# Kernel tuning notes

Hardware: AMD Instinct MI355X
Metric: run time of the kernel (lower is better)

The kernel has to match this reference:

```python
import jax, jax.numpy as jnp
import numpy as np

B, N, D = 16, 1024, 768
H = 12
HD = D // H           # 64
NUM_BUCKETS = 49      # iRPE 'product' buckets, shared across heads
SCALE = HD ** -0.5


def setup_inputs() -> dict:
    key = jax.random.key(0)
    k1, k2, k3, k4, k5, k6 = jax.random.split(key, 6)
    x = jax.random.normal(k1, (B, N, D), dtype=jnp.float32)
    qkv_w = jax.random.normal(k2, (3 * D, D), dtype=jnp.float32) * 0.02
    rpe_table = jax.random.normal(k3, (NUM_BUCKETS, HD), dtype=jnp.float32) * 0.02
    rp_bucket = jax.random.randint(k4, (N, N), 0, NUM_BUCKETS, dtype=jnp.int32)
    proj_w = jax.random.normal(k5, (D, D), dtype=jnp.float32) * 0.02
    proj_b = jax.random.normal(k6, (D,), dtype=jnp.float32) * 0.02
    return {"x": x, "qkv_w": qkv_w, "rpe_table": rpe_table,
            "rp_bucket": rp_bucket, "proj_w": proj_w, "proj_b": proj_b}


def reference(x, qkv_w, rpe_table, rp_bucket, proj_w, proj_b):
    b, n, d = x.shape
    # qkv projection (no bias), split into q,k,v of shape [B,H,N,HD]
    qkv = (x @ qkv_w.T).reshape(b, n, 3, H, HD)
    qkv = jnp.transpose(qkv, (2, 0, 3, 1, 4))
    q, k, v = qkv[0], qkv[1], qkv[2]
    q = q * SCALE
    # full attention scores [B,H,N,N]
    attn = jnp.einsum('bhid,bhjd->bhij', q, k)
    # iRPE contextual bias on keys: project q onto the bucket table, then
    # gather per relative-position bucket: bias[b,h,i,j] = (q @ W^T)[b,h,i,rp_bucket[i,j]]
    bias_all = jnp.einsum('bhid,cd->bhic', q, rpe_table)   # [B,H,N,num_buckets]
    bias = bias_all[:, :, jnp.arange(n)[:, None], rp_bucket]  # [B,H,N,N]
    attn = jax.nn.softmax(attn + bias, axis=-1)
    out = jnp.einsum('bhij,bhjd->bhid', attn, v)            # [B,H,N,HD]
    out = jnp.transpose(out, (0, 2, 1, 3)).reshape(b, n, d)
    return out @ proj_w.T + proj_b
```

## Files before the change

### kernel.cpp

```cpp
#include <hip/hip_runtime.h>

typedef short bf16x8 __attribute__((ext_vector_type(8)));
typedef float f32x4 __attribute__((ext_vector_type(4)));

#define QSCALE 0.1803368801111204f

__device__ __forceinline__ unsigned short f2bf(float f){
  unsigned u = __float_as_uint(f);
  u = (u + 0x7fffu + ((u >> 16) & 1u)) >> 16;
  return (unsigned short)u;
}
__device__ __forceinline__ f32x4 mfma16(bf16x8 a, bf16x8 b, f32x4 c){
  return __builtin_amdgcn_mfma_f32_16x16x32_bf16(a, b, c, 0, 0, 0);
}
__device__ __forceinline__ void gload_lds16(const void* g, void* l){
  __builtin_amdgcn_global_load_lds((__attribute__((address_space(1))) void*)(g),
                                   (__attribute__((address_space(3))) void*)(l), 16, 0, 0);
}
__device__ __forceinline__ unsigned cvt_pk_bf16(float lo, float hi){
  unsigned r;
  asm("v_cvt_pk_bf16_f32 %0, %1, %2" : "=v"(r) : "v"(lo), "v"(hi));
  return r;
}
__device__ __forceinline__ float exp2_fast(float x){
  float r;
  asm("v_exp_f32 %0, %1" : "=v"(r) : "v"(x));
  return r;
}

__global__ __launch_bounds__(256) void prep_kernel(
    const float* __restrict__ x, const float* __restrict__ qw,
    const float* __restrict__ pw, const int* __restrict__ rp,
    unsigned short* __restrict__ xb, unsigned short* __restrict__ wb,
    unsigned short* __restrict__ pwb, unsigned char* __restrict__ rp8){
  const int T1 = 3145728;
  const int T2 = T1 + 442368;
  const int T3 = T2 + 147456;
  const int T4 = T3 + 262144;
  for (int t = blockIdx.x * 256 + threadIdx.x; t < T4; t += gridDim.x * 256){
    if (t < T3){
      const float4* src; ushort4* dst; int off;
      if (t < T1){ src = (const float4*)x;  dst = (ushort4*)xb;  off = t; }
      else if (t < T2){ src = (const float4*)qw; dst = (ushort4*)wb;  off = t - T1; }
      else { src = (const float4*)pw; dst = (ushort4*)pwb; off = t - T2; }
      float4 v = src[off];
      ushort4 u;
      u.x = f2bf(v.x); u.y = f2bf(v.y); u.z = f2bf(v.z); u.w = f2bf(v.w);
      dst[off] = u;
    } else {
      int off = t - T3;
      int4 v = ((const int4*)rp)[off];
      int row = (off * 4) >> 10;
      int sw = (row & 7) << 4;
      uchar4 u;
      u.x = (unsigned char)((v.x << 1) ^ sw);
      u.y = (unsigned char)((v.y << 1) ^ sw);
      u.z = (unsigned char)((v.z << 1) ^ sw);
      u.w = (unsigned char)((v.w << 1) ^ sw);
      ((uchar4*)rp8)[off] = u;
    }
  }
}

__device__ __forceinline__ void gemm_core(
    const unsigned short* __restrict__ A, const unsigned short* __restrict__ Bm,
    int m0, int n0, int K, unsigned short* As, unsigned short* Bs,
    f32x4 (&acc)[4][4]){
  const int tid = threadIdx.x, lane = tid & 63, wave = tid >> 6;
  const int g = lane >> 4, r16 = lane & 15;
  const int wr = wave >> 1, wc = wave & 1;
  for (int k0 = 0; k0 < K; k0 += 32){
    __syncthreads();
    #pragma unroll
    for (int j = 0; j < 2; j++){
      int ci = j * 256 + tid;
      int row = ci >> 2, c = ci & 3;
      gload_lds16(A  + (size_t)(m0 + row) * K + k0 + c * 8,
                  (char*)As + (j * 256 + wave * 64) * 16);
      gload_lds16(Bm + (size_t)(n0 + row) * K + k0 + c * 8,
                  (char*)Bs + (j * 256 + wave * 64) * 16);
    }
    __syncthreads();
    bf16x8 a[4], b[4];
    #pragma unroll
    for (int mi = 0; mi < 4; mi++)
      a[mi] = *(const bf16x8*)((const char*)As + (wr * 64 + mi * 16 + r16) * 64 + g * 16);
    #pragma unroll
    for (int ni = 0; ni < 4; ni++)
      b[ni] = *(const bf16x8*)((const char*)Bs + (wc * 64 + ni * 16 + r16) * 64 + g * 16);
    #pragma unroll
    for (int mi = 0; mi < 4; mi++)
      #pragma unroll
      for (int ni = 0; ni < 4; ni++)
        acc[mi][ni] = mfma16(a[mi], b[ni], acc[mi][ni]);
  }
}

__global__ __launch_bounds__(256) void qkv_gemm(
    const unsigned short* __restrict__ xb, const unsigned short* __restrict__ wb,
    unsigned short* __restrict__ q_s, unsigned short* __restrict__ k_s,
    unsigned short* __restrict__ v_t){
  __shared__ __align__(16) unsigned short As[128 * 32];
  __shared__ __align__(16) unsigned short Bs[128 * 32];
  f32x4 acc[4][4];
  #pragma unroll
  for (int i = 0; i < 4; i++)
    #pragma unroll
    for (int j = 0; j < 4; j++){
      acc[i][j][0] = 0.f; acc[i][j][1] = 0.f; acc[i][j][2] = 0.f; acc[i][j][3] = 0.f;
    }
  const int m0 = blockIdx.y * 128, n0 = blockIdx.x * 128;
  gemm_core(xb, wb, m0, n0, 768, As, Bs, acc);

  const int lane = threadIdx.x & 63, wave = threadIdx.x >> 6;
  const int g = lane >> 4, r16 = lane & 15;
  const int wr = wave >> 1, wc = wave & 1;
  #pragma unroll
  for (int mi = 0; mi < 4; mi++){
    #pragma unroll
    for (int ni = 0; ni < 4; ni++){
      int gcol = n0 + wc * 64 + ni * 16 + r16;
      int sel = gcol / 768;
      int rem = gcol - sel * 768;
      int h = rem >> 6, hd = rem & 63;
      #pragma unroll
      for (int r = 0; r < 4; r++){
        int grow = m0 + wr * 64 + mi * 16 + 4 * g + r;
        int bb = grow >> 10, ii = grow & 1023;
        size_t base = ((size_t)(bb * 12 + h)) << 16;
        float v = acc[mi][ni][r];
        if (sel == 0)      q_s[base + ((size_t)ii << 6) + hd] = f2bf(v * QSCALE);
        else if (sel == 1) k_s[base + ((size_t)ii << 6) + hd] = f2bf(v);
        else               v_t[base + ((size_t)hd << 10) + ii] = f2bf(v);
      }
    }
  }
}

__global__ __launch_bounds__(256) void attn_kernel(
    const unsigned short* __restrict__ q_s, const unsigned short* __restrict__ k_s,
    const unsigned short* __restrict__ v_t, const unsigned char* __restrict__ rp8,
    const float* __restrict__ rpe, unsigned short* __restrict__ ao){
  __shared__ __align__(16) char smem[32768];
  const int tid = threadIdx.x, lane = tid & 63, w = tid >> 6;
  const int g = lane >> 4, r16 = lane & 15;
  const int qb = blockIdx.x, bh = blockIdx.y;
  const size_t bh_base = (size_t)bh << 16;

  const int i_loc = w * 16 + r16;
  const size_t qoff = bh_base + ((size_t)(qb * 64 + i_loc) << 6);
  bf16x8 qf0 = *(const bf16x8*)(q_s + qoff + g * 8);
  bf16x8 qf1 = *(const bf16x8*)(q_s + qoff + 32 + g * 8);

  char* bias_lds = smem + 24576;
  const int s16 = (r16 & 7) << 4;
  #pragma unroll
  for (int jt = 0; jt < 4; jt++){
    int crow = jt * 16 + r16;
    bf16x8 a0, a1;
    #pragma unroll
    for (int e = 0; e < 8; e++){ a0[e] = 0; a1[e] = 0; }
    if (crow < 49){
      const float* rr = rpe + crow * 64 + g * 8;
      float4 x0 = *(const float4*)(rr);
      float4 x1 = *(const float4*)(rr + 4);
      float4 y0 = *(const float4*)(rr + 32);
      float4 y1 = *(const float4*)(rr + 36);
      a0[0]=f2bf(x0.x); a0[1]=f2bf(x0.y); a0[2]=f2bf(x0.z); a0[3]=f2bf(x0.w);
      a0[4]=f2bf(x1.x); a0[5]=f2bf(x1.y); a0[6]=f2bf(x1.z); a0[7]=f2bf(x1.w);
      a1[0]=f2bf(y0.x); a1[1]=f2bf(y0.y); a1[2]=f2bf(y0.z); a1[3]=f2bf(y0.w);
      a1[4]=f2bf(y1.x); a1[5]=f2bf(y1.y); a1[6]=f2bf(y1.z); a1[7]=f2bf(y1.w);
    }
    f32x4 z = {0.f, 0.f, 0.f, 0.f};
    z = mfma16(a0, qf0, z);
    z = mfma16(a1, qf1, z);
    uint2 u; u.x = cvt_pk_bf16(z[0], z[1]); u.y = cvt_pk_bf16(z[2], z[3]);
    *(uint2*)(bias_lds + i_loc * 128 + ((jt * 32 + 8 * g) ^ s16)) = u;
  }

  unsigned short* ks = (unsigned short*)smem;
  unsigned short* vs = (unsigned short*)(smem + 8192);
  char* pbuf = smem + 16384 + w * 2048;
  const char* browb = bias_lds + i_loc * 128;

  const int ci0 = tid, ci1 = 256 + tid;
  const int row0 = ci0 >> 3, sc0 = (ci0 & 7) ^ (row0 & 7);
  const int row1 = ci1 >> 3, sc1 = (ci1 & 7) ^ (row1 & 7);
  const char* kp0 = (const char*)(k_s + bh_base) + row0 * 128 + sc0 * 16;
  const char* kp1 = (const char*)(k_s + bh_base) + row1 * 128 + sc1 * 16;
  const char* vp0 = (const char*)(v_t + bh_base) + row0 * 2048 + sc0 * 16;
  const char* vp1 = (const char*)(v_t + bh_base) + row1 * 2048 + sc1 * 16;
  char* kl0 = (char*)smem + w * 1024;
  char* kl1 = (char*)smem + 4096 + w * 1024;
  char* vl0 = (char*)smem + 8192 + w * 1024;
  char* vl1 = (char*)smem + 12288 + w * 1024;
  const unsigned char* rprow = rp8 + ((size_t)(qb * 64 + i_loc) << 10);

  f32x4 o[4];
  #pragma unroll
  for (int dt = 0; dt < 4; dt++){ o[dt][0]=0.f; o[dt][1]=0.f; o[dt][2]=0.f; o[dt][3]=0.f; }
  float m_i = -INFINITY, l_i = 0.f;

  for (int kb = 0; kb < 16; kb++){
    __syncthreads();
    gload_lds16(kp0, kl0);
    gload_lds16(kp1, kl1);
    gload_lds16(vp0, vl0);
    gload_lds16(vp1, vl1);
    kp0 += 8192; kp1 += 8192; vp0 += 128; vp1 += 128;
    __syncthreads();

    f32x4 st[4];
    #pragma unroll
    for (int jt = 0; jt < 4; jt++){
      int krow = jt * 16 + r16;
      int sw = (krow & 7) << 4;
      bf16x8 ka0 = *(const bf16x8*)((char*)ks + krow * 128 + ((g * 16) ^ sw));
      bf16x8 ka1 = *(const bf16x8*)((char*)ks + krow * 128 + ((64 + g * 16) ^ sw));
      f32x4 z = {0.f, 0.f, 0.f, 0.f};
      z = mfma16(ka0, qf0, z);
      z = mfma16(ka1, qf1, z);
      st[jt] = z;
    }
    #pragma unroll
    for (int jt = 0; jt < 4; jt++){
      unsigned bu = *(const unsigned*)(rprow + kb * 64 + jt * 16 + g * 4);
      st[jt][0] += __uint_as_float((unsigned)*(const unsigned short*)(browb + (bu & 0xff)) << 16);
      st[jt][1] += __uint_as_float((unsigned)*(const unsigned short*)(browb + ((bu >> 8) & 0xff)) << 16);
      st[jt][2] += __uint_as_float((unsigned)*(const unsigned short*)(browb + ((bu >> 16) & 0xff)) << 16);
      st[jt][3] += __uint_as_float((unsigned)*(const unsigned short*)(browb + (bu >> 24)) << 16);
    }
    float tmax = -INFINITY;
    #pragma unroll
    for (int jt = 0; jt < 4; jt++)
      tmax = fmaxf(tmax, fmaxf(fmaxf(st[jt][0], st[jt][1]), fmaxf(st[jt][2], st[jt][3])));
    tmax = fmaxf(tmax, __shfl_xor(tmax, 16));
    tmax = fmaxf(tmax, __shfl_xor(tmax, 32));
    const bool skip = __all(tmax <= m_i + 8.f);
    if (!skip){
      float mnew = fmaxf(m_i, tmax);
      float alpha = exp2_fast(m_i - mnew);
      m_i = mnew;
      l_i *= alpha;
      float af[4];
      #pragma unroll
      for (int r = 0; r < 4; r++) af[r] = __shfl(alpha, 4 * g + r);
      #pragma unroll
      for (int dt = 0; dt < 4; dt++){
        o[dt][0] *= af[0]; o[dt][1] *= af[1]; o[dt][2] *= af[2]; o[dt][3] *= af[3];
      }
    }
    #pragma unroll
    for (int jt = 0; jt < 4; jt++){
      float p0 = exp2_fast(st[jt][0] - m_i);
      float p1 = exp2_fast(st[jt][1] - m_i);
      float p2 = exp2_fast(st[jt][2] - m_i);
      float p3 = exp2_fast(st[jt][3] - m_i);
      l_i += (p0 + p1) + (p2 + p3);
      uint2 u; u.x = cvt_pk_bf16(p0, p1); u.y = cvt_pk_bf16(p2, p3);
      *(uint2*)(pbuf + r16 * 128 + ((jt * 32 + g * 8) ^ ((r16 & 7) << 4))) = u;
    }
    #pragma unroll
    for (int kt = 0; kt < 2; kt++){
      bf16x8 pa = *(const bf16x8*)(pbuf + r16 * 128 + ((kt * 64 + g * 16) ^ ((r16 & 7) << 4)));
      #pragma unroll
      for (int dt = 0; dt < 4; dt++){
        int vrow = dt * 16 + r16;
        bf16x8 vb = *(const bf16x8*)((char*)vs + vrow * 128 + ((kt * 64 + g * 16) ^ ((vrow & 7) << 4)));
        o[dt] = mfma16(pa, vb, o[dt]);
      }
    }
  }

  l_i += __shfl_xor(l_i, 16);
  l_i += __shfl_xor(l_i, 32);
  float lf[4];
  #pragma unroll
  for (int r = 0; r < 4; r++) lf[r] = 1.f / __shfl(l_i, 4 * g + r);
  const int bidx = bh / 12, h = bh - bidx * 12;
  #pragma unroll
  for (int dt = 0; dt < 4; dt++){
    int d = dt * 16 + r16;
    #pragma unroll
    for (int r = 0; r < 4; r++){
      int i = qb * 64 + w * 16 + 4 * g + r;
      ao[(size_t)(bidx * 1024 + i) * 768 + h * 64 + d] = f2bf(o[dt][r] * lf[r]);
    }
  }
}

__global__ __launch_bounds__(256) void proj_gemm(
    const unsigned short* __restrict__ aob, const unsigned short* __restrict__ pwb,
    const float* __restrict__ pb, float* __restrict__ out){
  __shared__ __align__(16) unsigned short As[128 * 32];
  __shared__ __align__(16) unsigned short Bs[128 * 32];
  f32x4 acc[4][4];
  #pragma unroll
  for (int i = 0; i < 4; i++)
    #pragma unroll
    for (int j = 0; j < 4; j++){
      acc[i][j][0] = 0.f; acc[i][j][1] = 0.f; acc[i][j][2] = 0.f; acc[i][j][3] = 0.f;
    }
  const int m0 = blockIdx.y * 128, n0 = blockIdx.x * 128;
  gemm_core(aob, pwb, m0, n0, 768, As, Bs, acc);

  const int lane = threadIdx.x & 63, wave = threadIdx.x >> 6;
  const int g = lane >> 4, r16 = lane & 15;
  const int wr = wave >> 1, wc = wave & 1;
  #pragma unroll
  for (int mi = 0; mi < 4; mi++){
    #pragma unroll
    for (int ni = 0; ni < 4; ni++){
      int gcol = n0 + wc * 64 + ni * 16 + r16;
      float bias = pb[gcol];
      #pragma unroll
      for (int r = 0; r < 4; r++){
        int grow = m0 + wr * 64 + mi * 16 + 4 * g + r;
        out[(size_t)grow * 768 + gcol] = acc[mi][ni][r] + bias;
      }
    }
  }
}

extern "C" void kernel_launch(void* const* d_in, const int* in_sizes, int n_in,
                              void* d_out, int out_size, void* d_ws, size_t ws_size,
                              hipStream_t stream){
  const float* x      = (const float*)d_in[0];
  const float* qkv_w  = (const float*)d_in[1];
  const float* rpe    = (const float*)d_in[2];
  const int*   rp     = (const int*)d_in[3];
  const float* proj_w = (const float*)d_in[4];
  const float* proj_b = (const float*)d_in[5];
  float* out = (float*)d_out;
  char* ws = (char*)d_ws;

  unsigned short* xb  = (unsigned short*)(ws);
  unsigned short* wb  = (unsigned short*)(ws + 25165824);
  unsigned short* pwb = (unsigned short*)(ws + 28704768);
  unsigned char*  rp8 = (unsigned char*) (ws + 29884416);
  unsigned short* q_s = (unsigned short*)(ws + 30932992);
  unsigned short* k_s = (unsigned short*)(ws + 56098816);
  unsigned short* v_t = (unsigned short*)(ws + 81264640);
  unsigned short* aob = (unsigned short*)(ws + 106430464);

  prep_kernel<<<2048, 256, 0, stream>>>(x, qkv_w, proj_w, rp, xb, wb, pwb, rp8);
  qkv_gemm<<<dim3(18, 128), 256, 0, stream>>>(xb, wb, q_s, k_s, v_t);
  attn_kernel<<<dim3(16, 192), 256, 0, stream>>>(q_s, k_s, v_t, rp8, rpe, aob);
  proj_gemm<<<dim3(6, 128), 256, 0, stream>>>(aob, pwb, proj_b, out);
}
```

Baseline: 311.3 us.

## Double-buffer K/V tiles in LDS to overlap loads with attention compute

Grows shared memory from 32KB to 48KB and splits the K/V staging area into two 16KB buffers. The next K/V tile is issued with global_load_lds into the spare buffer while the current tile is consumed, so there is one barrier per iteration instead of two. This aims to hide global load latency behind the QK^T, bias, softmax and PV work. The larger LDS footprint may reduce how many blocks fit per CU.

```diff
diff --git a/kernel.cpp b/kernel.cpp
--- a/kernel.cpp
+++ b/kernel.cpp
@@ -141,7 +141,7 @@
     const unsigned short* __restrict__ q_s, const unsigned short* __restrict__ k_s,
     const unsigned short* __restrict__ v_t, const unsigned char* __restrict__ rp8,
     const float* __restrict__ rpe, unsigned short* __restrict__ ao){
-  __shared__ __align__(16) char smem[32768];
+  __shared__ __align__(16) char smem[49152];
   const int tid = threadIdx.x, lane = tid & 63, w = tid >> 6;
   const int g = lane >> 4, r16 = lane & 15;
   const int qb = blockIdx.x, bh = blockIdx.y;
@@ -152,7 +152,7 @@
   bf16x8 qf0 = *(const bf16x8*)(q_s + qoff + g * 8);
   bf16x8 qf1 = *(const bf16x8*)(q_s + qoff + 32 + g * 8);
 
-  char* bias_lds = smem + 24576;
+  char* bias_lds = smem + 40960;
   const int s16 = (r16 & 7) << 4;
   #pragma unroll
   for (int jt = 0; jt < 4; jt++){
@@ -178,9 +178,7 @@
     *(uint2*)(bias_lds + i_loc * 128 + ((jt * 32 + 8 * g) ^ s16)) = u;
   }
 
-  unsigned short* ks = (unsigned short*)smem;
-  unsigned short* vs = (unsigned short*)(smem + 8192);
-  char* pbuf = smem + 16384 + w * 2048;
+  char* pbuf = smem + 32768 + w * 2048;
   const char* browb = bias_lds + i_loc * 128;
 
   const int ci0 = tid, ci1 = 256 + tid;
@@ -190,10 +188,8 @@
   const char* kp1 = (const char*)(k_s + bh_base) + row1 * 128 + sc1 * 16;
   const char* vp0 = (const char*)(v_t + bh_base) + row0 * 2048 + sc0 * 16;
   const char* vp1 = (const char*)(v_t + bh_base) + row1 * 2048 + sc1 * 16;
-  char* kl0 = (char*)smem + w * 1024;
-  char* kl1 = (char*)smem + 4096 + w * 1024;
-  char* vl0 = (char*)smem + 8192 + w * 1024;
-  char* vl1 = (char*)smem + 12288 + w * 1024;
+  const int kd0 = w * 1024, kd1 = 4096 + w * 1024;
+  const int vd0 = 8192 + w * 1024, vd1 = 12288 + w * 1024;
   const unsigned char* rprow = rp8 + ((size_t)(qb * 64 + i_loc) << 10);
 
   f32x4 o[4];
@@ -201,22 +197,34 @@
   for (int dt = 0; dt < 4; dt++){ o[dt][0]=0.f; o[dt][1]=0.f; o[dt][2]=0.f; o[dt][3]=0.f; }
   float m_i = -INFINITY, l_i = 0.f;
 
+  gload_lds16(kp0, smem + kd0);
+  gload_lds16(kp1, smem + kd1);
+  gload_lds16(vp0, smem + vd0);
+  gload_lds16(vp1, smem + vd1);
+  kp0 += 8192; kp1 += 8192; vp0 += 128; vp1 += 128;
+  __syncthreads();
+
+  int cur = 0;
   for (int kb = 0; kb < 16; kb++){
-    __syncthreads();
-    gload_lds16(kp0, kl0);
-    gload_lds16(kp1, kl1);
-    gload_lds16(vp0, vl0);
-    gload_lds16(vp1, vl1);
-    kp0 += 8192; kp1 += 8192; vp0 += 128; vp1 += 128;
-    __syncthreads();
+    if (kb < 15){
+      char* wbuf = smem + ((cur ^ 1) << 14);
+      gload_lds16(kp0, wbuf + kd0);
+      gload_lds16(kp1, wbuf + kd1);
+      gload_lds16(vp0, wbuf + vd0);
+      gload_lds16(vp1, wbuf + vd1);
+      kp0 += 8192; kp1 += 8192; vp0 += 128; vp1 += 128;
+    }
+    const char* rbuf = smem + (cur << 14);
+    const unsigned short* ks = (const unsigned short*)rbuf;
+    const unsigned short* vs = (const unsigned short*)(rbuf + 8192);
 
     f32x4 st[4];
     #pragma unroll
     for (int jt = 0; jt < 4; jt++){
       int krow = jt * 16 + r16;
       int sw = (krow & 7) << 4;
-      bf16x8 ka0 = *(const bf16x8*)((char*)ks + krow * 128 + ((g * 16) ^ sw));
-      bf16x8 ka1 = *(const bf16x8*)((char*)ks + krow * 128 + ((64 + g * 16) ^ sw));
+      bf16x8 ka0 = *(const bf16x8*)((const char*)ks + krow * 128 + ((g * 16) ^ sw));
+      bf16x8 ka1 = *(const bf16x8*)((const char*)ks + krow * 128 + ((64 + g * 16) ^ sw));
       f32x4 z = {0.f, 0.f, 0.f, 0.f};
       z = mfma16(ka0, qf0, z);
       z = mfma16(ka1, qf1, z);
@@ -266,10 +274,12 @@
       #pragma unroll
       for (int dt = 0; dt < 4; dt++){
         int vrow = dt * 16 + r16;
-        bf16x8 vb = *(const bf16x8*)((char*)vs + vrow * 128 + ((kt * 64 + g * 16) ^ ((vrow & 7) << 4)));
+        bf16x8 vb = *(const bf16x8*)((const char*)vs + vrow * 128 + ((kt * 64 + g * 16) ^ ((vrow & 7) << 4)));
         o[dt] = mfma16(pa, vb, o[dt]);
       }
     }
+    __syncthreads();
+    cur ^= 1;
   }
 
   l_i += __shfl_xor(l_i, 16);
```

New measurement: 324.9 us. +4.4%, slower.

## Widen GEMM K-tile with swizzled LDS and prefetch RPE bias in attention

Applied to the files above, without the earlier changes.

The shared GEMM core now stages 64-wide K tiles, with an XOR swizzle on the LDS layout, and runs two MFMA sub-steps per barrier pair. This halves the number of sync rounds and avoids LDS bank conflicts, at the cost of doubling LDS per block. The attention kernel software-pipelines the rp_bucket index loads and the bias-table lookups one key block ahead, so their latency is hidden behind the QK MFMAs. It also raises wave priority around the MFMA sections. The prefetch adds register pressure (16 extra bias values per thread) and could lower occupancy.

```diff
diff --git a/kernel.cpp b/kernel.cpp
--- a/kernel.cpp
+++ b/kernel.cpp
@@ -69,30 +69,38 @@
   const int tid = threadIdx.x, lane = tid & 63, wave = tid >> 6;
   const int g = lane >> 4, r16 = lane & 15;
   const int wr = wave >> 1, wc = wave & 1;
-  for (int k0 = 0; k0 < K; k0 += 32){
+  for (int k0 = 0; k0 < K; k0 += 64){
     __syncthreads();
     #pragma unroll
-    for (int j = 0; j < 2; j++){
+    for (int j = 0; j < 4; j++){
       int ci = j * 256 + tid;
-      int row = ci >> 2, c = ci & 3;
-      gload_lds16(A  + (size_t)(m0 + row) * K + k0 + c * 8,
+      int row = ci >> 3, c = ci & 7;
+      int sc = c ^ (row & 7);
+      gload_lds16(A  + (size_t)(m0 + row) * K + k0 + sc * 8,
                   (char*)As + (j * 256 + wave * 64) * 16);
-      gload_lds16(Bm + (size_t)(n0 + row) * K + k0 + c * 8,
+      gload_lds16(Bm + (size_t)(n0 + row) * K + k0 + sc * 8,
                   (char*)Bs + (j * 256 + wave * 64) * 16);
     }
     __syncthreads();
-    bf16x8 a[4], b[4];
-    #pragma unroll
-    for (int mi = 0; mi < 4; mi++)
-      a[mi] = *(const bf16x8*)((const char*)As + (wr * 64 + mi * 16 + r16) * 64 + g * 16);
-    #pragma unroll
-    for (int ni = 0; ni < 4; ni++)
-      b[ni] = *(const bf16x8*)((const char*)Bs + (wc * 64 + ni * 16 + r16) * 64 + g * 16);
-    #pragma unroll
-    for (int mi = 0; mi < 4; mi++)
-      #pragma unroll
-      for (int ni = 0; ni < 4; ni++)
-        acc[mi][ni] = mfma16(a[mi], b[ni], acc[mi][ni]);
+    #pragma unroll
+    for (int kk = 0; kk < 2; kk++){
+      bf16x8 a[4], b[4];
+      #pragma unroll
+      for (int mi = 0; mi < 4; mi++){
+        int row = wr * 64 + mi * 16 + r16;
+        a[mi] = *(const bf16x8*)((const char*)As + row * 128 + ((kk * 64 + g * 16) ^ ((row & 7) << 4)));
+      }
+      #pragma unroll
+      for (int ni = 0; ni < 4; ni++){
+        int row = wc * 64 + ni * 16 + r16;
+        b[ni] = *(const bf16x8*)((const char*)Bs + row * 128 + ((kk * 64 + g * 16) ^ ((row & 7) << 4)));
+      }
+      #pragma unroll
+      for (int mi = 0; mi < 4; mi++)
+        #pragma unroll
+        for (int ni = 0; ni < 4; ni++)
+          acc[mi][ni] = mfma16(a[mi], b[ni], acc[mi][ni]);
+    }
   }
 }
 
@@ -100,8 +108,8 @@
     const unsigned short* __restrict__ xb, const unsigned short* __restrict__ wb,
     unsigned short* __restrict__ q_s, unsigned short* __restrict__ k_s,
     unsigned short* __restrict__ v_t){
-  __shared__ __align__(16) unsigned short As[128 * 32];
-  __shared__ __align__(16) unsigned short Bs[128 * 32];
+  __shared__ __align__(16) unsigned short As[128 * 64];
+  __shared__ __align__(16) unsigned short Bs[128 * 64];
   f32x4 acc[4][4];
   #pragma unroll
   for (int i = 0; i < 4; i++)
@@ -201,6 +209,21 @@
   for (int dt = 0; dt < 4; dt++){ o[dt][0]=0.f; o[dt][1]=0.f; o[dt][2]=0.f; o[dt][3]=0.f; }
   float m_i = -INFINITY, l_i = 0.f;
 
+  unsigned buc[4];
+  #pragma unroll
+  for (int jt = 0; jt < 4; jt++)
+    buc[jt] = *(const unsigned*)(rprow + jt * 16 + g * 4);
+  __syncthreads();
+  unsigned bcur[16];
+  #pragma unroll
+  for (int jt = 0; jt < 4; jt++){
+    unsigned bu = buc[jt];
+    bcur[jt*4+0] = *(const unsigned short*)(browb + (bu & 0xff));
+    bcur[jt*4+1] = *(const unsigned short*)(browb + ((bu >> 8) & 0xff));
+    bcur[jt*4+2] = *(const unsigned short*)(browb + ((bu >> 16) & 0xff));
+    bcur[jt*4+3] = *(const unsigned short*)(browb + (bu >> 24));
+  }
+
   for (int kb = 0; kb < 16; kb++){
     __syncthreads();
     gload_lds16(kp0, kl0);
@@ -208,27 +231,45 @@
     gload_lds16(vp0, vl0);
     gload_lds16(vp1, vl1);
     kp0 += 8192; kp1 += 8192; vp0 += 128; vp1 += 128;
+    unsigned bun[4];
+    if (kb < 15){
+      #pragma unroll
+      for (int jt = 0; jt < 4; jt++)
+        bun[jt] = *(const unsigned*)(rprow + (kb + 1) * 64 + jt * 16 + g * 4);
+    }
     __syncthreads();
 
     f32x4 st[4];
+    __builtin_amdgcn_s_setprio(1);
     #pragma unroll
     for (int jt = 0; jt < 4; jt++){
       int krow = jt * 16 + r16;
       int sw = (krow & 7) << 4;
-      bf16x8 ka0 = *(const bf16x8*)((char*)ks + krow * 128 + ((g * 16) ^ sw));
-      bf16x8 ka1 = *(const bf16x8*)((char*)ks + krow * 128 + ((64 + g * 16) ^ sw));
+      bf16x8 ka0 = *(const bf16x8*)((const char*)ks + krow * 128 + ((g * 16) ^ sw));
+      bf16x8 ka1 = *(const bf16x8*)((const char*)ks + krow * 128 + ((64 + g * 16) ^ sw));
       f32x4 z = {0.f, 0.f, 0.f, 0.f};
       z = mfma16(ka0, qf0, z);
       z = mfma16(ka1, qf1, z);
       st[jt] = z;
     }
+    __builtin_amdgcn_s_setprio(0);
+    unsigned bnx[16];
+    if (kb < 15){
+      #pragma unroll
+      for (int jt = 0; jt < 4; jt++){
+        unsigned bu = bun[jt];
+        bnx[jt*4+0] = *(const unsigned short*)(browb + (bu & 0xff));
+        bnx[jt*4+1] = *(const unsigned short*)(browb + ((bu >> 8) & 0xff));
+        bnx[jt*4+2] = *(const unsigned short*)(browb + ((bu >> 16) & 0xff));
+        bnx[jt*4+3] = *(const unsigned short*)(browb + (bu >> 24));
+      }
+    }
     #pragma unroll
     for (int jt = 0; jt < 4; jt++){
-      unsigned bu = *(const unsigned*)(rprow + kb * 64 + jt * 16 + g * 4);
-      st[jt][0] += __uint_as_float((unsigned)*(const unsigned short*)(browb + (bu & 0xff)) << 16);
-      st[jt][1] += __uint_as_float((unsigned)*(const unsigned short*)(browb + ((bu >> 8) & 0xff)) << 16);
-      st[jt][2] += __uint_as_float((unsigned)*(const unsigned short*)(browb + ((bu >> 16) & 0xff)) << 16);
-      st[jt][3] += __uint_as_float((unsigned)*(const unsigned short*)(browb + (bu >> 24)) << 16);
+      st[jt][0] += __uint_as_float(bcur[jt*4+0] << 16);
+      st[jt][1] += __uint_as_float(bcur[jt*4+1] << 16);
+      st[jt][2] += __uint_as_float(bcur[jt*4+2] << 16);
+      st[jt][3] += __uint_as_float(bcur[jt*4+3] << 16);
     }
     float tmax = -INFINITY;
     #pragma unroll
@@ -260,15 +301,21 @@
       uint2 u; u.x = cvt_pk_bf16(p0, p1); u.y = cvt_pk_bf16(p2, p3);
       *(uint2*)(pbuf + r16 * 128 + ((jt * 32 + g * 8) ^ ((r16 & 7) << 4))) = u;
     }
+    __builtin_amdgcn_s_setprio(1);
     #pragma unroll
     for (int kt = 0; kt < 2; kt++){
       bf16x8 pa = *(const bf16x8*)(pbuf + r16 * 128 + ((kt * 64 + g * 16) ^ ((r16 & 7) << 4)));
       #pragma unroll
       for (int dt = 0; dt < 4; dt++){
         int vrow = dt * 16 + r16;
-        bf16x8 vb = *(const bf16x8*)((char*)vs + vrow * 128 + ((kt * 64 + g * 16) ^ ((vrow & 7) << 4)));
+        bf16x8 vb = *(const bf16x8*)((const char*)vs + vrow * 128 + ((kt * 64 + g * 16) ^ ((vrow & 7) << 4)));
         o[dt] = mfma16(pa, vb, o[dt]);
       }
+    }
+    __builtin_amdgcn_s_setprio(0);
+    if (kb < 15){
+      #pragma unroll
+      for (int t = 0; t < 16; t++) bcur[t] = bnx[t];
     }
   }
 
@@ -292,8 +339,8 @@
 __global__ __launch_bounds__(256) void proj_gemm(
     const unsigned short* __restrict__ aob, const unsigned short* __restrict__ pwb,
     const float* __restrict__ pb, float* __restrict__ out){
-  __shared__ __align__(16) unsigned short As[128 * 32];
-  __shared__ __align__(16) unsigned short Bs[128 * 32];
+  __shared__ __align__(16) unsigned short As[128 * 64];
+  __shared__ __align__(16) unsigned short Bs[128 * 64];
   f32x4 acc[4][4];
   #pragma unroll
   for (int i = 0; i < 4; i++)
```

Result: slower. 328.4 us (+5.5%).

## Split RPE bias projection into separate kernel and gather bias from global memory

Applied to the files above, without the earlier changes.

Moves the q·rpe_table bias projection out of the attention kernel into its own bias_gemm kernel, which writes a per-row 64-entry bf16 table into the reused xb workspace. The attention kernel then gathers bias values from global (cached) memory instead of a swizzled LDS region, which shrinks LDS to 24 KB and may raise occupancy. The bucket-index loads are hoisted before the barrier, and s_setprio is placed around the MFMA sections. The cost is an extra kernel launch, an extra global round trip for the bias table, and scattered per-lane global gathers that replace LDS reads.

```diff
diff --git a/kernel.cpp b/kernel.cpp
--- a/kernel.cpp
+++ b/kernel.cpp
@@ -50,13 +50,11 @@
     } else {
       int off = t - T3;
       int4 v = ((const int4*)rp)[off];
-      int row = (off * 4) >> 10;
-      int sw = (row & 7) << 4;
       uchar4 u;
-      u.x = (unsigned char)((v.x << 1) ^ sw);
-      u.y = (unsigned char)((v.y << 1) ^ sw);
-      u.z = (unsigned char)((v.z << 1) ^ sw);
-      u.w = (unsigned char)((v.w << 1) ^ sw);
+      u.x = (unsigned char)(v.x << 1);
+      u.y = (unsigned char)(v.y << 1);
+      u.z = (unsigned char)(v.z << 1);
+      u.w = (unsigned char)(v.w << 1);
       ((uchar4*)rp8)[off] = u;
     }
   }
@@ -137,23 +135,18 @@
   }
 }
 
-__global__ __launch_bounds__(256) void attn_kernel(
-    const unsigned short* __restrict__ q_s, const unsigned short* __restrict__ k_s,
-    const unsigned short* __restrict__ v_t, const unsigned char* __restrict__ rp8,
-    const float* __restrict__ rpe, unsigned short* __restrict__ ao){
-  __shared__ __align__(16) char smem[32768];
+__global__ __launch_bounds__(256) void bias_gemm(
+    const unsigned short* __restrict__ q_s, const float* __restrict__ rpe,
+    unsigned short* __restrict__ bg){
   const int tid = threadIdx.x, lane = tid & 63, w = tid >> 6;
   const int g = lane >> 4, r16 = lane & 15;
   const int qb = blockIdx.x, bh = blockIdx.y;
   const size_t bh_base = (size_t)bh << 16;
-
   const int i_loc = w * 16 + r16;
   const size_t qoff = bh_base + ((size_t)(qb * 64 + i_loc) << 6);
   bf16x8 qf0 = *(const bf16x8*)(q_s + qoff + g * 8);
   bf16x8 qf1 = *(const bf16x8*)(q_s + qoff + 32 + g * 8);
-
-  char* bias_lds = smem + 24576;
-  const int s16 = (r16 & 7) << 4;
+  unsigned short* orow = bg + ((((size_t)bh << 10) + qb * 64 + i_loc) << 6);
   #pragma unroll
   for (int jt = 0; jt < 4; jt++){
     int crow = jt * 16 + r16;
@@ -175,13 +168,29 @@
     z = mfma16(a0, qf0, z);
     z = mfma16(a1, qf1, z);
     uint2 u; u.x = cvt_pk_bf16(z[0], z[1]); u.y = cvt_pk_bf16(z[2], z[3]);
-    *(uint2*)(bias_lds + i_loc * 128 + ((jt * 32 + 8 * g) ^ s16)) = u;
-  }
+    *(uint2*)(orow + jt * 16 + 4 * g) = u;
+  }
+}
+
+__global__ __launch_bounds__(256) void attn_kernel(
+    const unsigned short* __restrict__ q_s, const unsigned short* __restrict__ k_s,
+    const unsigned short* __restrict__ v_t, const unsigned char* __restrict__ rp8,
+    const unsigned short* __restrict__ bg, unsigned short* __restrict__ ao){
+  __shared__ __align__(16) char smem[24576];
+  const int tid = threadIdx.x, lane = tid & 63, w = tid >> 6;
+  const int g = lane >> 4, r16 = lane & 15;
+  const int qb = blockIdx.x, bh = blockIdx.y;
+  const size_t bh_base = (size_t)bh << 16;
+
+  const int i_loc = w * 16 + r16;
+  const size_t qoff = bh_base + ((size_t)(qb * 64 + i_loc) << 6);
+  bf16x8 qf0 = *(const bf16x8*)(q_s + qoff + g * 8);
+  bf16x8 qf1 = *(const bf16x8*)(q_s + qoff + 32 + g * 8);
 
   unsigned short* ks = (unsigned short*)smem;
   unsigned short* vs = (unsigned short*)(smem + 8192);
   char* pbuf = smem + 16384 + w * 2048;
-  const char* browb = bias_lds + i_loc * 128;
+  const char* browb = (const char*)(bg + ((((size_t)bh << 10) + qb * 64 + i_loc) << 6));
 
   const int ci0 = tid, ci1 = 256 + tid;
   const int row0 = ci0 >> 3, sc0 = (ci0 & 7) ^ (row0 & 7);
@@ -208,27 +217,36 @@
     gload_lds16(vp0, vl0);
     gload_lds16(vp1, vl1);
     kp0 += 8192; kp1 += 8192; vp0 += 128; vp1 += 128;
+    unsigned bu0 = *(const unsigned*)(rprow + kb * 64 + g * 4);
+    unsigned bu1 = *(const unsigned*)(rprow + kb * 64 + 16 + g * 4);
+    unsigned bu2 = *(const unsigned*)(rprow + kb * 64 + 32 + g * 4);
+    unsigned bu3 = *(const unsigned*)(rprow + kb * 64 + 48 + g * 4);
     __syncthreads();
 
     f32x4 st[4];
+    __builtin_amdgcn_s_setprio(1);
     #pragma unroll
     for (int jt = 0; jt < 4; jt++){
       int krow = jt * 16 + r16;
       int sw = (krow & 7) << 4;
-      bf16x8 ka0 = *(const bf16x8*)((char*)ks + krow * 128 + ((g * 16) ^ sw));
-      bf16x8 ka1 = *(const bf16x8*)((char*)ks + krow * 128 + ((64 + g * 16) ^ sw));
+      bf16x8 ka0 = *(const bf16x8*)((const char*)ks + krow * 128 + ((g * 16) ^ sw));
+      bf16x8 ka1 = *(const bf16x8*)((const char*)ks + krow * 128 + ((64 + g * 16) ^ sw));
       f32x4 z = {0.f, 0.f, 0.f, 0.f};
       z = mfma16(ka0, qf0, z);
       z = mfma16(ka1, qf1, z);
       st[jt] = z;
     }
-    #pragma unroll
-    for (int jt = 0; jt < 4; jt++){
-      unsigned bu = *(const unsigned*)(rprow + kb * 64 + jt * 16 + g * 4);
-      st[jt][0] += __uint_as_float((unsigned)*(const unsigned short*)(browb + (bu & 0xff)) << 16);
-      st[jt][1] += __uint_as_float((unsigned)*(const unsigned short*)(browb + ((bu >> 8) & 0xff)) << 16);
-      st[jt][2] += __uint_as_float((unsigned)*(const unsigned short*)(browb + ((bu >> 16) & 0xff)) << 16);
-      st[jt][3] += __uint_as_float((unsigned)*(const unsigned short*)(browb + (bu >> 24)) << 16);
+    __builtin_amdgcn_s_setprio(0);
+    {
+      unsigned bus[4] = {bu0, bu1, bu2, bu3};
+      #pragma unroll
+      for (int jt = 0; jt < 4; jt++){
+        unsigned bu = bus[jt];
+        st[jt][0] += __uint_as_float((unsigned)*(const unsigned short*)(browb + (bu & 0xff)) << 16);
+        st[jt][1] += __uint_as_float((unsigned)*(const unsigned short*)(browb + ((bu >> 8) & 0xff)) << 16);
+        st[jt][2] += __uint_as_float((unsigned)*(const unsigned short*)(browb + ((bu >> 16) & 0xff)) << 16);
+        st[jt][3] += __uint_as_float((unsigned)*(const unsigned short*)(browb + (bu >> 24)) << 16);
+      }
     }
     float tmax = -INFINITY;
     #pragma unroll
@@ -260,16 +278,18 @@
       uint2 u; u.x = cvt_pk_bf16(p0, p1); u.y = cvt_pk_bf16(p2, p3);
       *(uint2*)(pbuf + r16 * 128 + ((jt * 32 + g * 8) ^ ((r16 & 7) << 4))) = u;
     }
+    __builtin_amdgcn_s_setprio(1);
     #pragma unroll
     for (int kt = 0; kt < 2; kt++){
       bf16x8 pa = *(const bf16x8*)(pbuf + r16 * 128 + ((kt * 64 + g * 16) ^ ((r16 & 7) << 4)));
       #pragma unroll
       for (int dt = 0; dt < 4; dt++){
         int vrow = dt * 16 + r16;
-        bf16x8 vb = *(const bf16x8*)((char*)vs + vrow * 128 + ((kt * 64 + g * 16) ^ ((vrow & 7) << 4)));
+        bf16x8 vb = *(const bf16x8*)((const char*)vs + vrow * 128 + ((kt * 64 + g * 16) ^ ((vrow & 7) << 4)));
         o[dt] = mfma16(pa, vb, o[dt]);
       }
     }
+    __builtin_amdgcn_s_setprio(0);
   }
 
   l_i += __shfl_xor(l_i, 16);
@@ -342,9 +362,11 @@
   unsigned short* k_s = (unsigned short*)(ws + 56098816);
   unsigned short* v_t = (unsigned short*)(ws + 81264640);
   unsigned short* aob = (unsigned short*)(ws + 106430464);
+  unsigned short* bg  = xb;
 
   prep_kernel<<<2048, 256, 0, stream>>>(x, qkv_w, proj_w, rp, xb, wb, pwb, rp8);
   qkv_gemm<<<dim3(18, 128), 256, 0, stream>>>(xb, wb, q_s, k_s, v_t);
-  attn_kernel<<<dim3(16, 192), 256, 0, stream>>>(q_s, k_s, v_t, rp8, rpe, aob);
+  bias_gemm<<<dim3(16, 192), 256, 0, stream>>>(q_s, rpe, bg);
+  attn_kernel<<<dim3(16, 192), 256, 0, stream>>>(q_s, k_s, v_t, rp8, bg, aob);
   proj_gemm<<<dim3(6, 128), 256, 0, stream>>>(aob, pwb, proj_b, out);
 }
```

Result: slower. 429.0 us (+37.8%).
